# Kernel optimization log

Measured on AMD Instinct MI355X. Metric: run time of the kernel, lower is better.

Reference implementation:

```python
import jax, jax.numpy as jnp
import numpy as np

N, E = 50000, 800000          # n_nodes, n_edges
IN_C, OUT_C = 128, 64         # in_channels, out_channels


def setup_inputs() -> dict:
    key = jax.random.key(0)
    ks = jax.random.split(key, 12)
    def w(k, i, o):
        return jax.random.normal(k, (i, o), jnp.float32) / np.float32(np.sqrt(i))
    return {
        "x": jax.random.normal(ks[0], (N, IN_C), jnp.float32),
        "edge_index": jax.random.randint(ks[1], (2, E), 0, N),
        "eps": jax.random.normal(ks[2], (N, OUT_C), jnp.float32),
        # encoder GCNConv1: in -> 2*out
        "W_e1": w(ks[3], IN_C, 2 * OUT_C), "b_e1": jnp.zeros((2 * OUT_C,), jnp.float32),
        # encoder GCNConv2: 2*out -> out
        "W_e2": w(ks[4], 2 * OUT_C, OUT_C), "b_e2": jnp.zeros((OUT_C,), jnp.float32),
        # fc_mu / fc_logvar: out -> out
        "W_mu": w(ks[5], OUT_C, OUT_C), "b_mu": jnp.zeros((OUT_C,), jnp.float32),
        "W_lv": w(ks[6], OUT_C, OUT_C), "b_lv": jnp.zeros((OUT_C,), jnp.float32),
        # decoder GCNConv1: out -> in
        "W_d1": w(ks[7], OUT_C, IN_C), "b_d1": jnp.zeros((IN_C,), jnp.float32),
        # decoder GCNConv2: in -> in
        "W_d2": w(ks[8], IN_C, IN_C), "b_d2": jnp.zeros((IN_C,), jnp.float32),
    }


def _gcn_norm(edge_index, n):
    # PyG gcn_norm: add self-loops, symmetric D^-1/2 A D^-1/2 normalization
    loop = jnp.arange(n)
    src = jnp.concatenate([edge_index[0], loop])
    dst = jnp.concatenate([edge_index[1], loop])
    deg = jax.ops.segment_sum(jnp.ones_like(dst, jnp.float32), dst, num_segments=n)
    dinv = jnp.where(deg > 0, deg ** -0.5, 0.0)
    norm = dinv[src] * dinv[dst]  # [E + N]
    return src, dst, norm


def _gcn_conv(x, W, b, src, dst, norm, n):
    h = x @ W                       # linear transform first (small channel dim)
    msg = h[src] * norm[:, None]    # gather + edge scaling
    return jax.ops.segment_sum(msg, dst, num_segments=n) + b  # scatter-add + bias


def reference(x, edge_index, eps, W_e1, b_e1, W_e2, b_e2, W_mu, b_mu, W_lv, b_lv, W_d1, b_d1, W_d2, b_d2):
    n = x.shape[0]
    src, dst, norm = _gcn_norm(edge_index, n)
    # encoder
    h = jax.nn.relu(_gcn_conv(x, W_e1, b_e1, src, dst, norm, n))
    h = _gcn_conv(h, W_e2, b_e2, src, dst, norm, n)
    mu = h @ W_mu + b_mu
    logvar = h @ W_lv + b_lv
    # reparameterize (training mode)
    z = mu + eps * jnp.exp(0.5 * logvar)
    # decoder
    d = jax.nn.relu(_gcn_conv(z, W_d1, b_d1, src, dst, norm, n))
    d = _gcn_conv(d, W_d2, b_d2, src, dst, norm, n)
    return (d, mu, logvar)
```

## Files before the change

### kernel.cpp

```cpp
#include <hip/hip_runtime.h>
#include <math.h>

typedef unsigned short u16;
typedef unsigned int u32;
typedef __attribute__((ext_vector_type(8))) short s16x8;
typedef __attribute__((ext_vector_type(4))) float f32x4;

__device__ __forceinline__ float bf2f(u16 u) { return __uint_as_float(((u32)u) << 16); }
__device__ __forceinline__ u16 f2bf(float f) {
    u32 u = __float_as_uint(f);
    return (u16)((u + 0x7fffu + ((u >> 16) & 1u)) >> 16);
}

union U4 { u32 u[4]; s16x8 v; };

__device__ __forceinline__ s16x8 pack_hi(f32x4 x0, f32x4 x1) {
    U4 r;
    r.u[0] = (__float_as_uint(x0.y) & 0xFFFF0000u) | (__float_as_uint(x0.x) >> 16);
    r.u[1] = (__float_as_uint(x0.w) & 0xFFFF0000u) | (__float_as_uint(x0.z) >> 16);
    r.u[2] = (__float_as_uint(x1.y) & 0xFFFF0000u) | (__float_as_uint(x1.x) >> 16);
    r.u[3] = (__float_as_uint(x1.w) & 0xFFFF0000u) | (__float_as_uint(x1.z) >> 16);
    return r.v;
}
__device__ __forceinline__ s16x8 pack_lo(f32x4 x0, f32x4 x1) {
    float e0 = x0.x - __uint_as_float(__float_as_uint(x0.x) & 0xFFFF0000u);
    float e1 = x0.y - __uint_as_float(__float_as_uint(x0.y) & 0xFFFF0000u);
    float e2 = x0.z - __uint_as_float(__float_as_uint(x0.z) & 0xFFFF0000u);
    float e3 = x0.w - __uint_as_float(__float_as_uint(x0.w) & 0xFFFF0000u);
    float e4 = x1.x - __uint_as_float(__float_as_uint(x1.x) & 0xFFFF0000u);
    float e5 = x1.y - __uint_as_float(__float_as_uint(x1.y) & 0xFFFF0000u);
    float e6 = x1.z - __uint_as_float(__float_as_uint(x1.z) & 0xFFFF0000u);
    float e7 = x1.w - __uint_as_float(__float_as_uint(x1.w) & 0xFFFF0000u);
    U4 r;
    r.u[0] = (__float_as_uint(e1) & 0xFFFF0000u) | (__float_as_uint(e0) >> 16);
    r.u[1] = (__float_as_uint(e3) & 0xFFFF0000u) | (__float_as_uint(e2) >> 16);
    r.u[2] = (__float_as_uint(e5) & 0xFFFF0000u) | (__float_as_uint(e4) >> 16);
    r.u[3] = (__float_as_uint(e7) & 0xFFFF0000u) | (__float_as_uint(e6) >> 16);
    return r.v;
}

#define BSHIFT 9
#define BSIZE 512
#define BCAP 10240

struct PackArgs { const float* w[6]; };


__device__ __forceinline__ void pack_body(const PackArgs& pa, u16* __restrict__ out, int g, int t) {
    const int Ks[6] = {128, 128, 64, 64, 64, 128};
    const int Ms[6] = {128, 64, 64, 64, 128, 128};
    const int Off[6] = {0, 16384, 24576, 28672, 32768, 40960};
    int s = g >> 6;
    int id = (g & 63) * 256 + t;
    int K = Ks[s], M = Ms[s];
    if (id >= K * M) return;
    int ms = (M == 128) ? 7 : 6;
    int k = id >> ms, c = id & (M - 1);
    int chunk = k >> 5, j = k & 7, lq = (k >> 3) & 3;
    int ct = c >> 4, ln = (c & 15) + (lq << 4);
    out[Off[s] + (chunk * (M >> 4) + ct) * 512 + ln * 8 + j] = f2bf(pa.w[s][id]);
}


__global__ __launch_bounds__(256) void k_bin_pack(const int* __restrict__ ei, int E, int NB, int C,
                                                  int* __restrict__ bin_cursor, u32* __restrict__ binned,
                                                  PackArgs pa, u16* __restrict__ wpk) {
    __shared__ int sh[256];
    const int t = threadIdx.x;
    if ((int)blockIdx.x >= C) {
        pack_body(pa, wpk, blockIdx.x - C, t);
        return;
    }
    int* hist = sh;
    int* base_l = sh + 128;
    const int e0 = blockIdx.x * 4096;
    int sreg[16], dreg[16];
#pragma unroll
    for (int j = 0; j < 16; ++j) {
        int e = e0 + j * 256 + t;
        if (e < E) {
            sreg[j] = ei[e];
            dreg[j] = ei[E + e];
        } else {
            dreg[j] = -1;
        }
    }
    if (t < NB) hist[t] = 0;
    __syncthreads();
#pragma unroll
    for (int j = 0; j < 16; ++j)
        if (dreg[j] >= 0) atomicAdd(&hist[dreg[j] >> BSHIFT], 1);
    __syncthreads();
    if (t < NB) {
        base_l[t] = atomicAdd(&bin_cursor[t], hist[t]);
        hist[t] = 0;
    }
    __syncthreads();
#pragma unroll
    for (int j = 0; j < 16; ++j)
        if (dreg[j] >= 0) {
            int b = dreg[j] >> BSHIFT;
            int pos = base_l[b] + atomicAdd(&hist[b], 1);
            if (pos < BCAP) binned[(size_t)b * BCAP + pos] = ((u32)(dreg[j] & (BSIZE - 1)) << 17) | (u32)sreg[j];
        }
}


template <int K, int M, int RT, int NSET, bool XBF16, bool OUT_BF16, bool BREL>
__device__ __forceinline__ void gemm_tile(const void* __restrict__ Xv, const u16* __restrict__ Bpk,
                                          const float* __restrict__ b0, const float* __restrict__ b1,
                                          const float* __restrict__ eps,
                                          void* __restrict__ Y0, float* __restrict__ Y1,
                                          u16* __restrict__ Z, int N, int col0, int row0, int t) {
    constexpr int CH = K / 32;
    constexpr int TPM = M >> 4;
    constexpr int SETSTRIDE = CH * TPM * 512;
    const int lane = t & 63, w = t >> 6;
    const int l15 = lane & 15, q = lane >> 4;

    s16x8 Bfr[NSET * CH * 4];
#pragma unroll
    for (int s = 0; s < NSET; ++s)
#pragma unroll
        for (int ch = 0; ch < CH; ++ch)
#pragma unroll
            for (int ct = 0; ct < 4; ++ct)
                Bfr[(s * CH + ch) * 4 + ct] =
                    *(const s16x8*)&Bpk[(size_t)s * SETSTRIDE + ((ch * TPM) + (col0 >> 4) + ct) * 512 + lane * 8];

    f32x4 acc[NSET][RT][4];
#pragma unroll
    for (int s = 0; s < NSET; ++s)
#pragma unroll
        for (int rt = 0; rt < RT; ++rt)
#pragma unroll
            for (int ct = 0; ct < 4; ++ct) acc[s][rt][ct] = 0.f;

#pragma unroll
    for (int ch = 0; ch < CH; ++ch) {
#pragma unroll
        for (int rt = 0; rt < RT; ++rt) {
            int r = row0 + (w * RT + rt) * 16 + l15;
            r = r < N ? r : N - 1;
            s16x8 ah, al;
            if (XBF16) {
                ah = *(const s16x8*)((const u16*)Xv + (size_t)r * K + (ch << 5) + (q << 3));
            } else {
                const float* xp = (const float*)Xv + (size_t)r * K + (ch << 5) + (q << 3);
                f32x4 x0 = *(const f32x4*)xp;
                f32x4 x1 = *(const f32x4*)(xp + 4);
                ah = pack_hi(x0, x1);
                al = pack_lo(x0, x1);
            }
#pragma unroll
            for (int s = 0; s < NSET; ++s)
#pragma unroll
                for (int ct = 0; ct < 4; ++ct) {
                    int fb = (s * CH + ch) * 4 + ct;
                    acc[s][rt][ct] = __builtin_amdgcn_mfma_f32_16x16x32_bf16(ah, Bfr[fb], acc[s][rt][ct], 0, 0, 0);
                    if (!XBF16)
                        acc[s][rt][ct] = __builtin_amdgcn_mfma_f32_16x16x32_bf16(al, Bfr[fb], acc[s][rt][ct], 0, 0, 0);
                }
        }
    }

#pragma unroll
    for (int rt = 0; rt < RT; ++rt)
#pragma unroll
        for (int ct = 0; ct < 4; ++ct)
#pragma unroll
            for (int reg = 0; reg < 4; ++reg) {
                int row = row0 + (w * RT + rt) * 16 + q * 4 + reg;
                if (row >= N) continue;
                int col = col0 + ct * 16 + l15;
                if (NSET == 1) {
                    float v = acc[0][rt][ct][reg];
                    if (BREL) v = fmaxf(v + b0[col], 0.f);
                    if (OUT_BF16)
                        ((u16*)Y0)[(size_t)row * M + col] = f2bf(v);
                    else
                        ((float*)Y0)[(size_t)row * M + col] = v;
                } else {
                    float mu = acc[0][rt][ct][reg] + b0[col];
                    float lv = acc[1][rt][ct][reg] + b1[col];
                    size_t o = (size_t)row * 64 + col;
                    ((float*)Y0)[o] = mu;
                    Y1[o] = lv;
                    Z[o] = f2bf(mu + eps[o] * expf(0.5f * lv));
                }
            }
}

template <int K, int M, int RT, int NSET, bool XBF16, bool OUT_BF16, bool BREL>
__global__ __launch_bounds__(256, 3) void k_gemm(const void* __restrict__ Xv, const u16* __restrict__ Bpk,
                                                 const float* __restrict__ b0, const float* __restrict__ b1,
                                                 const float* __restrict__ eps,
                                                 void* __restrict__ Y0, float* __restrict__ Y1,
                                                 u16* __restrict__ Z, int N) {
    gemm_tile<K, M, RT, NSET, XBF16, OUT_BF16, BREL>(Xv, Bpk, b0, b1, eps, Y0, Y1, Z, N,
                                                     blockIdx.x * 64, blockIdx.y * (RT * 64), threadIdx.x);
}


__global__ __launch_bounds__(256, 3) void k_cnt_gemm1(const u32* __restrict__ binned,
                                                      const int* __restrict__ bin_cursor, int N, int NB,
                                                      int* __restrict__ cnt, float* __restrict__ dinv,
                                                      int* __restrict__ row_start, int* __restrict__ cursor,
                                                      const float* __restrict__ x, const u16* __restrict__ wpk,
                                                      u16* __restrict__ R1) {
    __shared__ int cnt_l[BSIZE];
    __shared__ int wave_sum[5];
    __shared__ int base_s;
    const int t = threadIdx.x;
    const int b = blockIdx.x;
    if (b >= NB) {
        gemm_tile<128, 128, 2, 1, false, true, false>(x, wpk, nullptr, nullptr, nullptr, R1, nullptr, nullptr,
                                                      N, 0, (b - NB) * 128, t);
        return;
    }
    const int lane = t & 63, w = t >> 6;
    cnt_l[t] = 0;
    cnt_l[t + 256] = 0;
    __syncthreads();
    const int n = min(bin_cursor[b], BCAP);
    for (int i = t; i < n; i += 256) atomicAdd(&cnt_l[binned[(size_t)b * BCAP + i] >> 17], 1);
    __syncthreads();
    int c0 = cnt_l[2 * t], c1 = cnt_l[2 * t + 1];
    int p0 = (c0 + 7) & ~7, p1 = (c1 + 7) & ~7;
    int s = p0 + p1;
    int incl = s;
#pragma unroll
    for (int o = 1; o < 64; o <<= 1) {
        int v = __shfl_up(incl, o, 64);
        if (lane >= o) incl += v;
    }
    if (lane == 63) wave_sum[w] = incl;
    __syncthreads();
    if (t == 0) {
        int acc = 0;
#pragma unroll
        for (int i = 0; i < 4; ++i) {
            int v = wave_sum[i];
            wave_sum[i] = acc;
            acc += v;
        }
        base_s = atomicAdd(cursor, acc);
    }
    __syncthreads();
    int excl = incl - s + wave_sum[w] + base_s;
    int v0 = b * BSIZE + 2 * t;
    if (v0 < N) {
        cnt[v0] = c0;
        dinv[v0] = rsqrtf((float)(c0 + 1));
        row_start[v0] = excl;
    }
    if (v0 + 1 < N) {
        cnt[v0 + 1] = c1;
        dinv[v0 + 1] = rsqrtf((float)(c1 + 1));
        row_start[v0 + 1] = excl + p0;
    }
}


__global__ __launch_bounds__(256, 3) void k_scat_gemm1(const u32* __restrict__ binned,
                                                       const int* __restrict__ bin_cursor,
                                                       const int* __restrict__ row_start,
                                                       const float* __restrict__ dinv, int N, int NB,
                                                       int2* __restrict__ edges,
                                                       const float* __restrict__ x, const u16* __restrict__ wpk,
                                                       u16* __restrict__ R1) {
    __shared__ float dv_l[BSIZE];
    __shared__ int rs_l[BSIZE];
    __shared__ int fill_l[BSIZE];
    const int t = threadIdx.x;
    const int b = blockIdx.x;
    if (b >= NB) {
        gemm_tile<128, 128, 2, 1, false, true, false>(x, wpk, nullptr, nullptr, nullptr, R1, nullptr, nullptr,
                                                      N, 64, (b - NB) * 128, t);
        return;
    }
#pragma unroll
    for (int hh = 0; hh < 2; ++hh) {
        int d = t + hh * 256;
        int v = b * BSIZE + d;
        bool ok = v < N;
        dv_l[d] = ok ? dinv[v] : 0.f;
        rs_l[d] = ok ? row_start[v] : 0;
        fill_l[d] = 0;
    }
    __syncthreads();
    const int n = min(bin_cursor[b], BCAP);
    for (int i = t; i < n; i += 256) {
        u32 e = binned[(size_t)b * BCAP + i];
        int dl = e >> 17;
        int src = e & 0x1FFFF;
        float wgt = dinv[src] * dv_l[dl];
        int pos = rs_l[dl] + atomicAdd(&fill_l[dl], 1);
        edges[pos] = make_int2(src, __float_as_int(wgt));
    }
    __syncthreads();
#pragma unroll
    for (int hh = 0; hh < 2; ++hh) {
        int d = t + hh * 256;
        int v = b * BSIZE + d;
        if (v >= N) continue;
        int c = fill_l[d];
        int pc = (c + 7) & ~7;
        for (int j = c; j < pc; ++j) edges[rs_l[d] + j] = make_int2(0, 0);
    }
}


template <int CHU, int SL, bool RELU, bool OUT_BF16, bool HASB>
__global__ __launch_bounds__(256) void k_aggs(const u16* __restrict__ hin, const int2* __restrict__ edges,
                                              const int* __restrict__ row_start, const int* __restrict__ cnt,
                                              const float* __restrict__ dinv, const float* __restrict__ bias,
                                              void* __restrict__ out, int N) {
    const int t = threadIdx.x;
    const int w = t >> 6, l = t & 63;
    const int sub = l >> 4, li = l & 15;
    const int slice = (int)blockIdx.x % SL;
    const int g = (int)blockIdx.x / SL;
    const int v = g * 16 + w * 4 + sub;
    const int off = slice * 16 + li;
    const u32* hp = (const u32*)hin;
    const bool ok = v < N;
    int start = 0, pc = 0;
    if (ok) {
        start = row_start[v];
        pc = (cnt[v] + 7) & ~7;
    }
    float a0 = 0.f, a1 = 0.f;
    for (int i = 0; i < pc; i += 8) {
        int2 e[8];
#pragma unroll
        for (int j = 0; j < 8; ++j) e[j] = edges[start + i + j];
        u32 h[8];
#pragma unroll
        for (int j = 0; j < 8; ++j) h[j] = hp[(u32)e[j].x * CHU + off];
#pragma unroll
        for (int j = 0; j < 8; ++j) {
            float wv = __int_as_float(e[j].y);
            a0 = fmaf(wv, __uint_as_float(h[j] << 16), a0);
            a1 = fmaf(wv, __uint_as_float(h[j] & 0xFFFF0000u), a1);
        }
    }
    if (!ok) return;
    float dv = dinv[v], sw = dv * dv;
    u32 hs = hp[(u32)v * CHU + off];
    a0 = fmaf(sw, __uint_as_float(hs << 16), a0);
    a1 = fmaf(sw, __uint_as_float(hs & 0xFFFF0000u), a1);
    if (HASB) {
        float2 bp = ((const float2*)bias)[off];
        a0 += bp.x;
        a1 += bp.y;
    }
    if (RELU) {
        a0 = fmaxf(a0, 0.f);
        a1 = fmaxf(a1, 0.f);
    }
    if (OUT_BF16)
        ((u32*)out)[(size_t)v * CHU + off] = (u32)f2bf(a0) | ((u32)f2bf(a1) << 16);
    else
        ((float2*)out)[(size_t)v * CHU + off] = make_float2(a0, a1);
}


extern "C" void kernel_launch(void* const* d_in, const int* in_sizes, int n_in,
                              void* d_out, int out_size, void* d_ws, size_t ws_size,
                              hipStream_t stream) {
    const float* x = (const float*)d_in[0];
    const int* ei = (const int*)d_in[1];
    const float* eps = (const float*)d_in[2];
    const float* We1 = (const float*)d_in[3];
    const float* be1 = (const float*)d_in[4];
    const float* We2 = (const float*)d_in[5];
    const float* be2 = (const float*)d_in[6];
    const float* Wmu = (const float*)d_in[7];
    const float* bmu = (const float*)d_in[8];
    const float* Wlv = (const float*)d_in[9];
    const float* blv = (const float*)d_in[10];
    const float* Wd1 = (const float*)d_in[11];
    const float* bd1 = (const float*)d_in[12];
    const float* Wd2 = (const float*)d_in[13];
    const float* bd2 = (const float*)d_in[14];

    const int N = in_sizes[0] / 128;
    const int E = in_sizes[1] / 2;
    const int ECAP = E + 8 * N;
    const int NB = (N + BSIZE - 1) >> BSHIFT;
    const int C = (E + 4095) / 4096;

    int* bin_cursor = (int*)d_ws;
    int* cursor = bin_cursor + 128;
    float* dinv = (float*)(bin_cursor + 256);
    int* row_start = (int*)(dinv + N);
    int* cnt = row_start + N;
    int2* edges = (int2*)(cnt + N);
    u16* R1 = (u16*)(edges + ECAP);
    u16* AZu = R1 + (size_t)N * 128;
    u16* B2 = AZu + (size_t)N * 128;
    u16* Wpk = B2 + (size_t)N * 128;
    float* AZf = (float*)AZu;
    u32* binned = (u32*)AZu;

    float* out_d = (float*)d_out;
    float* out_mu = out_d + (size_t)N * 128;
    float* out_lv = out_mu + (size_t)N * 64;
    float* H2 = out_d;

    hipMemsetAsync(d_ws, 0, 256 * 4, stream);

    PackArgs pa;
    pa.w[0] = We1; pa.w[1] = We2; pa.w[2] = Wmu; pa.w[3] = Wlv; pa.w[4] = Wd1; pa.w[5] = Wd2;

    const int RB128 = (N + 127) / 128;
    const int RB64 = (N + 63) / 64;
    const int GB = (N + 15) / 16;

    k_bin_pack<<<dim3(C + 384), dim3(256), 0, stream>>>(ei, E, NB, C, bin_cursor, binned, pa, Wpk);
    k_cnt_gemm1<<<dim3(NB + RB128), dim3(256), 0, stream>>>(binned, bin_cursor, N, NB, cnt, dinv, row_start,
                                                            cursor, x, Wpk, R1);
    k_scat_gemm1<<<dim3(NB + RB128), dim3(256), 0, stream>>>(binned, bin_cursor, row_start, dinv, N, NB,
                                                             edges, x, Wpk, R1);
    k_aggs<64, 4, true, true, true><<<dim3(4 * GB), dim3(256), 0, stream>>>(R1, edges, row_start, cnt, dinv, be1, AZu, N);
    k_gemm<128, 64, 1, 1, true, true, false><<<dim3(1, RB64), dim3(256), 0, stream>>>(AZu, Wpk + 16384, nullptr, nullptr, nullptr, R1, nullptr, nullptr, N);
    k_aggs<32, 2, false, false, true><<<dim3(2 * GB), dim3(256), 0, stream>>>(R1, edges, row_start, cnt, dinv, be2, H2, N);
    k_gemm<64, 64, 1, 2, false, false, false><<<dim3(1, RB64), dim3(256), 0, stream>>>(H2, Wpk + 24576, bmu, blv, eps, out_mu, out_lv, R1, N);
    k_aggs<32, 2, false, false, false><<<dim3(2 * GB), dim3(256), 0, stream>>>(R1, edges, row_start, cnt, dinv, nullptr, AZf, N);
    k_gemm<64, 128, 2, 1, false, true, true><<<dim3(2, RB128), dim3(256), 0, stream>>>(AZf, Wpk + 32768, bd1, nullptr, nullptr, B2, nullptr, nullptr, N);
    k_gemm<128, 128, 2, 1, true, true, false><<<dim3(2, RB128), dim3(256), 0, stream>>>(B2, Wpk + 40960, nullptr, nullptr, nullptr, R1, nullptr, nullptr, N);
    k_aggs<64, 4, false, false, true><<<dim3(4 * GB), dim3(256), 0, stream>>>(R1, edges, row_start, cnt, dinv, bd2, out_d, N);
}
```

Baseline: 342.5 us.

## Pin aggregation column slices to XCDs with persistent atomic work queues

The aggregation kernel becomes persistent, launched with a fixed 2048 blocks. Each block reads its XCD id from a hardware register and picks a channel slice from it, so each XCD's L2 only caches that slice of the gathered feature matrix instead of every slice. Blocks take 16-node groups from a per-slice atomic counter, which also gives dynamic load balancing. The cost is one atomic and two block barriers per group, a larger workspace memset, and a dependence on the hardware spreading blocks across XCDs.

```diff
diff --git a/kernel.cpp b/kernel.cpp
--- a/kernel.cpp
+++ b/kernel.cpp
@@ -315,54 +315,64 @@
 __global__ __launch_bounds__(256) void k_aggs(const u16* __restrict__ hin, const int2* __restrict__ edges,
                                               const int* __restrict__ row_start, const int* __restrict__ cnt,
                                               const float* __restrict__ dinv, const float* __restrict__ bias,
-                                              void* __restrict__ out, int N) {
+                                              void* __restrict__ out, int N, int* __restrict__ cur) {
+    __shared__ int s_g;
     const int t = threadIdx.x;
     const int w = t >> 6, l = t & 63;
     const int sub = l >> 4, li = l & 15;
-    const int slice = (int)blockIdx.x % SL;
-    const int g = (int)blockIdx.x / SL;
-    const int v = g * 16 + w * 4 + sub;
+    int xcd;
+    asm("s_getreg_b32 %0, hwreg(HW_REG_XCC_ID, 0, 32)" : "=s"(xcd));
+    const int slice = xcd & (SL - 1);
     const int off = slice * 16 + li;
+    const int GB = (N + 15) >> 4;
     const u32* hp = (const u32*)hin;
-    const bool ok = v < N;
-    int start = 0, pc = 0;
-    if (ok) {
-        start = row_start[v];
-        pc = (cnt[v] + 7) & ~7;
-    }
-    float a0 = 0.f, a1 = 0.f;
-    for (int i = 0; i < pc; i += 8) {
-        int2 e[8];
-#pragma unroll
-        for (int j = 0; j < 8; ++j) e[j] = edges[start + i + j];
-        u32 h[8];
-#pragma unroll
-        for (int j = 0; j < 8; ++j) h[j] = hp[(u32)e[j].x * CHU + off];
-#pragma unroll
-        for (int j = 0; j < 8; ++j) {
-            float wv = __int_as_float(e[j].y);
-            a0 = fmaf(wv, __uint_as_float(h[j] << 16), a0);
-            a1 = fmaf(wv, __uint_as_float(h[j] & 0xFFFF0000u), a1);
-        }
-    }
-    if (!ok) return;
-    float dv = dinv[v], sw = dv * dv;
-    u32 hs = hp[(u32)v * CHU + off];
-    a0 = fmaf(sw, __uint_as_float(hs << 16), a0);
-    a1 = fmaf(sw, __uint_as_float(hs & 0xFFFF0000u), a1);
-    if (HASB) {
-        float2 bp = ((const float2*)bias)[off];
-        a0 += bp.x;
-        a1 += bp.y;
-    }
-    if (RELU) {
-        a0 = fmaxf(a0, 0.f);
-        a1 = fmaxf(a1, 0.f);
-    }
-    if (OUT_BF16)
-        ((u32*)out)[(size_t)v * CHU + off] = (u32)f2bf(a0) | ((u32)f2bf(a1) << 16);
-    else
-        ((float2*)out)[(size_t)v * CHU + off] = make_float2(a0, a1);
+    for (;;) {
+        if (t == 0) s_g = atomicAdd(cur + slice, 1);
+        __syncthreads();
+        const int g = s_g;
+        __syncthreads();
+        if (g >= GB) break;
+        const int v = g * 16 + w * 4 + sub;
+        const bool ok = v < N;
+        int start = 0, pc = 0;
+        if (ok) {
+            start = row_start[v];
+            pc = (cnt[v] + 7) & ~7;
+        }
+        float a0 = 0.f, a1 = 0.f;
+        for (int i = 0; i < pc; i += 8) {
+            int2 e[8];
+#pragma unroll
+            for (int j = 0; j < 8; ++j) e[j] = edges[start + i + j];
+            u32 h[8];
+#pragma unroll
+            for (int j = 0; j < 8; ++j) h[j] = hp[(size_t)(u32)e[j].x * CHU + off];
+#pragma unroll
+            for (int j = 0; j < 8; ++j) {
+                float wv = __int_as_float(e[j].y);
+                a0 = fmaf(wv, __uint_as_float(h[j] << 16), a0);
+                a1 = fmaf(wv, __uint_as_float(h[j] & 0xFFFF0000u), a1);
+            }
+        }
+        if (!ok) continue;
+        float dv = dinv[v], sw = dv * dv;
+        u32 hs = hp[(size_t)v * CHU + off];
+        a0 = fmaf(sw, __uint_as_float(hs << 16), a0);
+        a1 = fmaf(sw, __uint_as_float(hs & 0xFFFF0000u), a1);
+        if (HASB) {
+            float2 bp = ((const float2*)bias)[off];
+            a0 += bp.x;
+            a1 += bp.y;
+        }
+        if (RELU) {
+            a0 = fmaxf(a0, 0.f);
+            a1 = fmaxf(a1, 0.f);
+        }
+        if (OUT_BF16)
+            ((u32*)out)[(size_t)v * CHU + off] = (u32)f2bf(a0) | ((u32)f2bf(a1) << 16);
+        else
+            ((float2*)out)[(size_t)v * CHU + off] = make_float2(a0, a1);
+    }
 }
 
 
@@ -393,7 +403,8 @@
 
     int* bin_cursor = (int*)d_ws;
     int* cursor = bin_cursor + 128;
-    float* dinv = (float*)(bin_cursor + 256);
+    int* agg_cur = bin_cursor + 256;
+    float* dinv = (float*)(bin_cursor + 512);
     int* row_start = (int*)(dinv + N);
     int* cnt = row_start + N;
     int2* edges = (int2*)(cnt + N);
@@ -409,26 +420,26 @@
     float* out_lv = out_mu + (size_t)N * 64;
     float* H2 = out_d;
 
-    hipMemsetAsync(d_ws, 0, 256 * 4, stream);
+    hipMemsetAsync(d_ws, 0, 2048, stream);
 
     PackArgs pa;
     pa.w[0] = We1; pa.w[1] = We2; pa.w[2] = Wmu; pa.w[3] = Wlv; pa.w[4] = Wd1; pa.w[5] = Wd2;
 
     const int RB128 = (N + 127) / 128;
     const int RB64 = (N + 63) / 64;
-    const int GB = (N + 15) / 16;
+    const int AGB = 2048;
 
     k_bin_pack<<<dim3(C + 384), dim3(256), 0, stream>>>(ei, E, NB, C, bin_cursor, binned, pa, Wpk);
     k_cnt_gemm1<<<dim3(NB + RB128), dim3(256), 0, stream>>>(binned, bin_cursor, N, NB, cnt, dinv, row_start,
                                                             cursor, x, Wpk, R1);
     k_scat_gemm1<<<dim3(NB + RB128), dim3(256), 0, stream>>>(binned, bin_cursor, row_start, dinv, N, NB,
                                                              edges, x, Wpk, R1);
-    k_aggs<64, 4, true, true, true><<<dim3(4 * GB), dim3(256), 0, stream>>>(R1, edges, row_start, cnt, dinv, be1, AZu, N);
+    k_aggs<64, 4, true, true, true><<<dim3(AGB), dim3(256), 0, stream>>>(R1, edges, row_start, cnt, dinv, be1, AZu, N, agg_cur + 0);
     k_gemm<128, 64, 1, 1, true, true, false><<<dim3(1, RB64), dim3(256), 0, stream>>>(AZu, Wpk + 16384, nullptr, nullptr, nullptr, R1, nullptr, nullptr, N);
-    k_aggs<32, 2, false, false, true><<<dim3(2 * GB), dim3(256), 0, stream>>>(R1, edges, row_start, cnt, dinv, be2, H2, N);
+    k_aggs<32, 2, false, false, true><<<dim3(AGB), dim3(256), 0, stream>>>(R1, edges, row_start, cnt, dinv, be2, H2, N, agg_cur + 8);
     k_gemm<64, 64, 1, 2, false, false, false><<<dim3(1, RB64), dim3(256), 0, stream>>>(H2, Wpk + 24576, bmu, blv, eps, out_mu, out_lv, R1, N);
-    k_aggs<32, 2, false, false, false><<<dim3(2 * GB), dim3(256), 0, stream>>>(R1, edges, row_start, cnt, dinv, nullptr, AZf, N);
+    k_aggs<32, 2, false, false, false><<<dim3(AGB), dim3(256), 0, stream>>>(R1, edges, row_start, cnt, dinv, nullptr, AZf, N, agg_cur + 16);
     k_gemm<64, 128, 2, 1, false, true, true><<<dim3(2, RB128), dim3(256), 0, stream>>>(AZf, Wpk + 32768, bd1, nullptr, nullptr, B2, nullptr, nullptr, N);
     k_gemm<128, 128, 2, 1, true, true, false><<<dim3(2, RB128), dim3(256), 0, stream>>>(B2, Wpk + 40960, nullptr, nullptr, nullptr, R1, nullptr, nullptr, N);
-    k_aggs<64, 4, false, false, true><<<dim3(4 * GB), dim3(256), 0, stream>>>(R1, edges, row_start, cnt, dinv, bd2, out_d, N);
-}
+    k_aggs<64, 4, false, false, true><<<dim3(AGB), dim3(256), 0, stream>>>(R1, edges, row_start, cnt, dinv, bd2, out_d, N, agg_cur + 24);
+}
```

New measurement: 761.9 us. 2.22x slower.
